# Kernel optimization log

Hardware: AMD Instinct MI355X
Metric: run time of the kernel (lower is better)

## Reference

```python
import jax, jax.numpy as jnp
import numpy as np

# Module constants derived from default grid_config
D = 59          # depth bins: (60-1)/1
C_OUT = 64
X, Y, Z = 128, 128, 7
STRIDE = 16
GRID_LB = np.array([-51.2, -51.2, -2.5], dtype=np.float32)
GRID_IV = np.array([0.8, 0.8, 1.0], dtype=np.float32)
D0, DSTEP = 1.0, 1.0

B, N, C_IN, H, W = 4, 6, 256, 16, 44


def _voxel_coords():
    xs, ys, zs = np.meshgrid(np.arange(X), np.arange(Y), np.arange(Z), indexing='ij')
    coords = np.stack([xs, ys, zs], axis=-1).reshape(-1, 3).astype(np.float32)
    coords = coords * GRID_IV + GRID_LB  # [V, 3] ego-frame voxel centers
    return coords


def _camera_rig(rng):
    """Realistic 6-camera rig: yawed cameras looking outward, z_cam = forward."""
    c2e = np.zeros((B, N, 4, 4), dtype=np.float32)
    K = np.zeros((B, N, 3, 3), dtype=np.float32)
    for b in range(B):
        for n in range(N):
            a = 2.0 * np.pi * n / N + 0.02 * rng.standard_normal()
            f = np.array([np.cos(a), np.sin(a), 0.0])           # camera forward (z_cam)
            x_cam = np.array([-np.sin(a), np.cos(a), 0.0])      # camera right
            y_cam = np.array([0.0, 0.0, -1.0])                   # camera down
            R = np.stack([x_cam, y_cam, f], axis=1)              # columns = cam axes in ego
            t = 1.0 * f + np.array([0.0, 0.0, 1.5])
            c2e[b, n, :3, :3] = R
            c2e[b, n, :3, 3] = t
            c2e[b, n, 3, 3] = 1.0
            fl = 400.0 + 5.0 * rng.standard_normal()
            K[b, n] = np.array([[fl, 0.0, 352.0], [0.0, fl, 128.0], [0.0, 0.0, 1.0]])
    return c2e, K


def setup_inputs() -> dict:
    key = jax.random.key(0)
    k1, k2, k3 = jax.random.split(key, 3)
    img_feats = jax.random.normal(k1, (B, N, C_IN, H, W), dtype=jnp.float32)
    c2e, K = _camera_rig(np.random.default_rng(0))
    # depth_net: 1x1 conv in_channels -> D + C_OUT
    w_depth = jax.random.normal(k2, (D + C_OUT, C_IN), dtype=jnp.float32) * (1.0 / np.sqrt(C_IN))
    b_depth = jax.random.normal(k3, (D + C_OUT,), dtype=jnp.float32) * 0.01
    return {
        'img_feats': img_feats,
        'cam2ego': jnp.asarray(c2e),
        'cam_intrinsics': jnp.asarray(K),
        'w_depth': w_depth,
        'b_depth': b_depth,
    }


def reference(img_feats, cam2ego, cam_intrinsics, w_depth, b_depth):
    Bc, Nc, C, Hc, Wc = img_feats.shape
    # 1x1 conv == per-pixel linear
    x = jnp.einsum('bnchw,oc->bnhwo', img_feats, w_depth) + b_depth  # [B,N,H,W,D+C_OUT]
    depth = jax.nn.softmax(x[..., :D], axis=-1)                      # [B,N,H,W,D]
    feat = x[..., D:]                                                # [B,N,H,W,C_OUT]

    vox = jnp.asarray(_voxel_coords())                               # [V,3]
    V = vox.shape[0]
    vox_h = jnp.concatenate([vox, jnp.ones((V, 1), vox.dtype)], axis=1)  # [V,4]

    e2c = jnp.linalg.inv(cam2ego)                                    # [B,N,4,4]
    cam = jnp.einsum('bnij,vj->bnvi', e2c, vox_h)[..., :3]           # [B,N,V,3]
    z = cam[..., 2]
    z_safe = jnp.maximum(z, 0.1)
    norm = cam[..., :2] / z_safe[..., None]
    homo = jnp.concatenate([norm, jnp.ones_like(z[..., None])], axis=-1)  # [B,N,V,3]
    img = jnp.einsum('bnij,bnvj->bnvi', cam_intrinsics, homo)[..., :2]
    fc = img / STRIDE                                                # feature-plane coords

    depth_bin = ((z - D0) / DSTEP).astype(jnp.int32)                 # trunc toward 0, matches .long()
    valid = (
        (fc[..., 0] >= 0) & (fc[..., 0] < Wc)
        & (fc[..., 1] >= 0) & (fc[..., 1] < Hc)
        & (z > 0.5)
        & (depth_bin >= 0) & (depth_bin < D)
    )

    u = jnp.clip(fc[..., 0].astype(jnp.int32), 0, Wc - 1)            # [B,N,V]
    v = jnp.clip(fc[..., 1].astype(jnp.int32), 0, Hc - 1)
    d = jnp.clip(depth_bin, 0, D - 1)
    hw = v * Wc + u

    feat_flat = feat.reshape(Bc, Nc, Hc * Wc, C_OUT)
    sampled_feat = jnp.take_along_axis(feat_flat, hw[..., None], axis=2)   # [B,N,V,C_OUT]
    depth_flat = depth.reshape(Bc, Nc, Hc * Wc * D)
    sampled_depth = jnp.take_along_axis(depth_flat, hw * D + d, axis=2)    # [B,N,V]

    wgt = sampled_depth * valid.astype(sampled_depth.dtype)
    # scatter_add at flat_idx == voxel index (identity) -> masked sum over cameras
    bev = jnp.einsum('bnv,bnvc->bvc', wgt, sampled_feat)             # [B,V,C_OUT]
    bev = bev.reshape(Bc, X, Y, Z, C_OUT).sum(axis=3)                # collapse Z
    bev = bev.transpose(0, 3, 2, 1)                                  # [B,C_OUT,Y,X]
    return bev, depth
```

## Files before the change

kernel.cpp:

```cpp
#include <hip/hip_runtime.h>
#include <math.h>

#define D_BINS 59
#define CO     64
#define CI     256
#define NB     4
#define NC     6
#define H_IMG  16
#define W_IMG  44
#define HW     704
#define NPIX   (NB*NC*HW)
#define XD     128
#define YD     128
#define ZD     7
#define NOUT   123
#define PXB    66

typedef float v2f __attribute__((ext_vector_type(2)));

__device__ void inv_rigid(const float* __restrict__ M, float* __restrict__ o) {
    double a = M[0], b = M[1], c = M[2], t0 = M[3];
    double d = M[4], e = M[5], f = M[6], t1 = M[7];
    double g = M[8], h = M[9], ii = M[10], t2 = M[11];
    double A00 = e*ii - f*h, A01 = c*h - b*ii, A02 = b*f - c*e;
    double A10 = f*g - d*ii, A11 = a*ii - c*g, A12 = c*d - a*f;
    double A20 = d*h - e*g,  A21 = b*g - a*h,  A22 = a*e - b*d;
    double det = a*A00 + b*A10 + c*A20;
    double inv = 1.0 / det;
    double r00 = A00*inv, r01 = A01*inv, r02 = A02*inv;
    double r10 = A10*inv, r11 = A11*inv, r12 = A12*inv;
    double r20 = A20*inv, r21 = A21*inv, r22 = A22*inv;
    o[0] = (float)r00; o[1] = (float)r01; o[2]  = (float)r02;
    o[3] = (float)(-(r00*t0 + r01*t1 + r02*t2));
    o[4] = (float)r10; o[5] = (float)r11; o[6]  = (float)r12;
    o[7] = (float)(-(r10*t0 + r11*t1 + r12*t2));
    o[8] = (float)r20; o[9] = (float)r21; o[10] = (float)r22;
    o[11] = (float)(-(r20*t0 + r21*t1 + r22*t2));
}

__global__ __launch_bounds__(256) void k_pre(
    const float* __restrict__ wd, const float* __restrict__ c2e,
    float* __restrict__ wt2, float* __restrict__ e2c) {
    const int o = blockIdx.x;
    const int k = threadIdx.x;
    float v = (o < NOUT) ? wd[(size_t)o * CI + k] : 0.f;
    wt2[(size_t)(k >> 1) * 256 + o * 2 + (k & 1)] = v;
    if (blockIdx.x == 0 && k < NB * NC)
        inv_rigid(c2e + k * 16, e2c + k * 12);
}

__global__ __launch_bounds__(640) void k_head(
    const float* __restrict__ img, const float* __restrict__ wt2,
    const float* __restrict__ bd, float* __restrict__ depth_out,
    float* __restrict__ feat_ws) {
    __shared__ float smem[PXB * 132 + PXB];
    float* S = smem + PXB * 132;

    const int tid = threadIdx.x;
    const int wv  = tid >> 6;
    const int ln  = tid & 63;
    const int p0  = blockIdx.x * PXB;
    const bool is_main = (wv < 8);
    const int o0  = __builtin_amdgcn_readfirstlane((is_main ? wv : 0) << 4);
    const int epx = 64 + (wv - 8);

    v2f acc[16];
#pragma unroll
    for (int j = 0; j < 16; ++j) acc[j] = (v2f)(0.f);
    v2f acc2a = (v2f)(0.f), acc2b = (v2f)(0.f);

    for (int kc = 0; kc < 4; ++kc) {
#pragma unroll
        for (int it = 0; it < 7; ++it) {
            int idx = tid + it * 640;
            if (idx < 64 * PXB) {
                int kl = idx / PXB, px = idx - kl * PXB;
                int p = p0 + px;
                int bn = p / HW, hw = p - bn * HW;
                smem[(kl >> 1) * 132 + px * 2 + (kl & 1)] =
                    img[((size_t)bn * CI + kc * 64 + kl) * HW + hw];
            }
        }
        __syncthreads();
        if (is_main) {
#pragma unroll 4
            for (int k2 = 0; k2 < 32; ++k2) {
                v2f a = *(const v2f*)(smem + k2 * 132 + ln * 2);
                const v2f* w =
                    (const v2f*)(wt2 + (size_t)(kc * 32 + k2) * 256) + o0;
#pragma unroll
                for (int j = 0; j < 16; ++j)
                    acc[j] = __builtin_elementwise_fma(a, w[j], acc[j]);
            }
        } else {
#pragma unroll 4
            for (int k2 = 0; k2 < 32; ++k2) {
                v2f a = *(const v2f*)(smem + k2 * 132 + epx * 2);
                const float* w = wt2 + (size_t)(kc * 32 + k2) * 256;
                v2f w0 = {w[ln * 2], w[ln * 2 + 1]};
                v2f w1 = {w[(ln + 64) * 2], w[(ln + 64) * 2 + 1]};
                acc2a = __builtin_elementwise_fma(a, w0, acc2a);
                acc2b = __builtin_elementwise_fma(a, w1, acc2b);
            }
        }
        __syncthreads();
    }

    float* X = smem;
    if (is_main) {
#pragma unroll
        for (int j = 0; j < 16; ++j) {
            int o = o0 + j;
            if (o < NOUT) {
                int col = (o < D_BINS) ? o : o + 5;
                X[ln * 132 + col] = (acc[j].x + acc[j].y) + bd[o];
            }
        }
    } else {
        int o = ln;
        X[epx * 132 + ((o < D_BINS) ? o : o + 5)] = (acc2a.x + acc2a.y) + bd[o];
        o = ln + 64;
        if (o < NOUT)
            X[epx * 132 + ((o < D_BINS) ? o : o + 5)] = (acc2b.x + acc2b.y) + bd[o];
    }
    __syncthreads();

#pragma unroll
    for (int it = 0; it < 2; ++it) {
        int g = tid + it * 640;
        if (g < PXB * 16) {
            int p = g >> 4, m = g & 15;
            float4 v = *(const float4*)(X + p * 132 + 64 + m * 4);
            *(float4*)(feat_ws + (size_t)(p0 + p) * CO + m * 4) = v;
        }
    }

    if (tid < PXB) {
        float* row = X + tid * 132;
        float m = row[0];
        for (int o = 1; o < D_BINS; ++o) m = fmaxf(m, row[o]);
        float s = 0.f;
        for (int o = 0; o < D_BINS; ++o) {
            float e = __expf(row[o] - m);
            row[o] = e;
            s += e;
        }
        S[tid] = 1.f / s;
    }
    __syncthreads();

    for (int g = tid; g < PXB * D_BINS; g += 640) {
        int p = g / D_BINS;
        int o = g - p * D_BINS;
        depth_out[(size_t)p0 * D_BINS + g] = X[p * 132 + o] * S[p];
    }
}

__global__ __launch_bounds__(256) void k_splat(
    const float* __restrict__ e2c, const float* __restrict__ Kmat,
    const float* __restrict__ depth_g, const float* __restrict__ feat_ws,
    float* __restrict__ bev) {
    __shared__ int   hw_s[ZD][64];
    __shared__ float wgt_s[ZD][64];

    const int tx = threadIdx.x;
    const int cq = threadIdx.y;
    const int x = blockIdx.x * 64 + tx;
    const int y = blockIdx.y;
    const int b = blockIdx.z;
    const float wx = (float)x * 0.8f + (-51.2f);
    const float wy = (float)y * 0.8f + (-51.2f);

    float acc[16];
#pragma unroll
    for (int m = 0; m < 16; ++m) acc[m] = 0.f;

    for (int n = 0; n < NC; ++n) {
        const int bn = b * NC + n;
        const float* E = e2c + bn * 12;
        const float* Km = Kmat + bn * 9;
        const float k00 = Km[0], k01 = Km[1], k02 = Km[2];
        const float k10 = Km[3], k11 = Km[4], k12 = Km[5];
        const float e02 = E[2], e12 = E[6], e22 = E[10];
        const float bx0 = E[0] * wx + E[1] * wy + E[3];
        const float bx1 = E[4] * wx + E[5] * wy + E[7];
        const float bx2 = E[8] * wx + E[9] * wy + E[11];

#pragma unroll
        for (int zz = 0; zz < 2; ++zz) {
            const int z = cq + zz * 4;
            if (z < ZD) {
                const float wz = -2.5f + (float)z;
                const float cx = bx0 + e02 * wz;
                const float cy = bx1 + e12 * wz;
                const float cz = bx2 + e22 * wz;
                const float zs = fmaxf(cz, 0.1f);
                const float rz = 1.0f / zs;
                const float xn = cx * rz;
                const float yn = cy * rz;
                const float fu = (k00 * xn + k01 * yn + k02) * 0.0625f;
                const float fv = (k10 * xn + k11 * yn + k12) * 0.0625f;
                const int bin = (int)(cz - 1.0f);
                const bool valid = (fu >= 0.f) & (fu < (float)W_IMG) &
                                   (fv >= 0.f) & (fv < (float)H_IMG) &
                                   (cz > 0.5f) & (bin >= 0) & (bin < D_BINS);
                int hw = -1;
                float wgt = 0.f;
                if (valid) {
                    int u = (int)fu;
                    int v = (int)fv;
                    hw = v * W_IMG + u;
                    wgt = depth_g[((size_t)bn * HW + hw) * D_BINS + bin];
                }
                hw_s[z][tx] = hw;
                wgt_s[z][tx] = wgt;
            }
        }
        __syncthreads();

#pragma unroll
        for (int z = 0; z < ZD; ++z) {
            const int hw = hw_s[z][tx];
            if (hw >= 0) {
                const float wgt = wgt_s[z][tx];
                const float4* fp =
                    (const float4*)(feat_ws + ((size_t)bn * HW + hw) * CO + cq * 16);
                float4 f0 = fp[0], f1 = fp[1], f2 = fp[2], f3 = fp[3];
                acc[0]  = fmaf(wgt, f0.x, acc[0]);
                acc[1]  = fmaf(wgt, f0.y, acc[1]);
                acc[2]  = fmaf(wgt, f0.z, acc[2]);
                acc[3]  = fmaf(wgt, f0.w, acc[3]);
                acc[4]  = fmaf(wgt, f1.x, acc[4]);
                acc[5]  = fmaf(wgt, f1.y, acc[5]);
                acc[6]  = fmaf(wgt, f1.z, acc[6]);
                acc[7]  = fmaf(wgt, f1.w, acc[7]);
                acc[8]  = fmaf(wgt, f2.x, acc[8]);
                acc[9]  = fmaf(wgt, f2.y, acc[9]);
                acc[10] = fmaf(wgt, f2.z, acc[10]);
                acc[11] = fmaf(wgt, f2.w, acc[11]);
                acc[12] = fmaf(wgt, f3.x, acc[12]);
                acc[13] = fmaf(wgt, f3.y, acc[13]);
                acc[14] = fmaf(wgt, f3.z, acc[14]);
                acc[15] = fmaf(wgt, f3.w, acc[15]);
            }
        }
        __syncthreads();
    }
    float* ob = bev + (((size_t)b * CO + cq * 16) * YD + y) * XD + x;
#pragma unroll
    for (int m = 0; m < 16; ++m) ob[(size_t)m * YD * XD] = acc[m];
}

extern "C" void kernel_launch(void* const* d_in, const int* in_sizes, int n_in,
                              void* d_out, int out_size, void* d_ws, size_t ws_size,
                              hipStream_t stream) {
    const float* img  = (const float*)d_in[0];
    const float* c2e  = (const float*)d_in[1];
    const float* Kmat = (const float*)d_in[2];
    const float* wd   = (const float*)d_in[3];
    const float* bd   = (const float*)d_in[4];
    float* bev = (float*)d_out;
    float* depth_out = bev + (size_t)NB * CO * YD * XD;
    float* feat_ws = (float*)d_ws;
    float* wt2 = feat_ws + (size_t)NPIX * CO;
    float* e2c = wt2 + 128 * 256;

    k_pre<<<128, 256, 0, stream>>>(wd, c2e, wt2, e2c);
    k_head<<<256, 640, 0, stream>>>(img, wt2, bd, depth_out, feat_ws);
    k_splat<<<dim3(2, YD, NB), dim3(64, 4, 1), 0, stream>>>(e2c, Kmat, depth_out,
                                                            feat_ws, bev);
}
```

Baseline: 124.0 us.

## Retile depth-head GEMM into 32-pixel blocks with split-K across waves

Rewrites the 1x1-conv head kernel to process 32 pixels per 256-thread block, loading all 256 input channels into shared memory at once. Each lane owns two output channels and sixteen pixels, and two wave pairs split the K dimension, reducing their partials through LDS. The grid grows from 256 to 528 blocks for better CU coverage, and the irregular 66-pixel tile with special-case extra waves is removed. In exchange there is more weight traffic per pixel from global memory and a larger shared-memory footprint.

```diff
diff --git a/kernel.cpp b/kernel.cpp
--- a/kernel.cpp
+++ b/kernel.cpp
@@ -14,7 +14,8 @@
 #define YD     128
 #define ZD     7
 #define NOUT   123
-#define PXB    66
+#define PXT    32
+#define XW     132
 
 typedef float v2f __attribute__((ext_vector_type(2)));
 
@@ -49,94 +50,83 @@
         inv_rigid(c2e + k * 16, e2c + k * 12);
 }
 
-__global__ __launch_bounds__(640) void k_head(
+__global__ __launch_bounds__(256) void k_head(
     const float* __restrict__ img, const float* __restrict__ wt2,
     const float* __restrict__ bd, float* __restrict__ depth_out,
     float* __restrict__ feat_ws) {
-    __shared__ float smem[PXB * 132 + PXB];
-    float* S = smem + PXB * 132;
+    __shared__ float A[128 * 64];
+    __shared__ float Xs[PXT * XW];
+    __shared__ float S[PXT];
 
     const int tid = threadIdx.x;
     const int wv  = tid >> 6;
     const int ln  = tid & 63;
-    const int p0  = blockIdx.x * PXB;
-    const bool is_main = (wv < 8);
-    const int o0  = __builtin_amdgcn_readfirstlane((is_main ? wv : 0) << 4);
-    const int epx = 64 + (wv - 8);
-
-    v2f acc[16];
-#pragma unroll
-    for (int j = 0; j < 16; ++j) acc[j] = (v2f)(0.f);
-    v2f acc2a = (v2f)(0.f), acc2b = (v2f)(0.f);
-
-    for (int kc = 0; kc < 4; ++kc) {
-#pragma unroll
-        for (int it = 0; it < 7; ++it) {
-            int idx = tid + it * 640;
-            if (idx < 64 * PXB) {
-                int kl = idx / PXB, px = idx - kl * PXB;
-                int p = p0 + px;
-                int bn = p / HW, hw = p - bn * HW;
-                smem[(kl >> 1) * 132 + px * 2 + (kl & 1)] =
-                    img[((size_t)bn * CI + kc * 64 + kl) * HW + hw];
-            }
-        }
-        __syncthreads();
-        if (is_main) {
-#pragma unroll 4
-            for (int k2 = 0; k2 < 32; ++k2) {
-                v2f a = *(const v2f*)(smem + k2 * 132 + ln * 2);
-                const v2f* w =
-                    (const v2f*)(wt2 + (size_t)(kc * 32 + k2) * 256) + o0;
-#pragma unroll
-                for (int j = 0; j < 16; ++j)
-                    acc[j] = __builtin_elementwise_fma(a, w[j], acc[j]);
-            }
-        } else {
-#pragma unroll 4
-            for (int k2 = 0; k2 < 32; ++k2) {
-                v2f a = *(const v2f*)(smem + k2 * 132 + epx * 2);
-                const float* w = wt2 + (size_t)(kc * 32 + k2) * 256;
-                v2f w0 = {w[ln * 2], w[ln * 2 + 1]};
-                v2f w1 = {w[(ln + 64) * 2], w[(ln + 64) * 2 + 1]};
-                acc2a = __builtin_elementwise_fma(a, w0, acc2a);
-                acc2b = __builtin_elementwise_fma(a, w1, acc2b);
-            }
-        }
-        __syncthreads();
-    }
-
-    float* X = smem;
-    if (is_main) {
-#pragma unroll
-        for (int j = 0; j < 16; ++j) {
-            int o = o0 + j;
-            if (o < NOUT) {
-                int col = (o < D_BINS) ? o : o + 5;
-                X[ln * 132 + col] = (acc[j].x + acc[j].y) + bd[o];
-            }
-        }
-    } else {
-        int o = ln;
-        X[epx * 132 + ((o < D_BINS) ? o : o + 5)] = (acc2a.x + acc2a.y) + bd[o];
-        o = ln + 64;
-        if (o < NOUT)
-            X[epx * 132 + ((o < D_BINS) ? o : o + 5)] = (acc2b.x + acc2b.y) + bd[o];
-    }
-    __syncthreads();
-
-#pragma unroll
-    for (int it = 0; it < 2; ++it) {
-        int g = tid + it * 640;
-        if (g < PXB * 16) {
-            int p = g >> 4, m = g & 15;
-            float4 v = *(const float4*)(X + p * 132 + 64 + m * 4);
-            *(float4*)(feat_ws + (size_t)(p0 + p) * CO + m * 4) = v;
-        }
-    }
-
-    if (tid < PXB) {
-        float* row = X + tid * 132;
+    const int p0  = blockIdx.x * PXT;
+    const int pw0 = (wv & 1) << 4;
+    const int kh  = wv >> 1;
+    const int kb  = __builtin_amdgcn_readfirstlane(kh << 6);
+
+    const int bn  = p0 / HW;
+    const int hw0 = p0 - bn * HW;
+    const float* gsrc = img + (size_t)bn * CI * HW + hw0;
+#pragma unroll 8
+    for (int it = 0; it < 32; ++it) {
+        int idx = tid + it * 256;
+        int ch = idx >> 5, px = idx & 31;
+        A[(ch >> 1) * 64 + px * 2 + (ch & 1)] = gsrc[ch * HW + px];
+    }
+    __syncthreads();
+
+    v2f accA[16], accB[16];
+#pragma unroll
+    for (int p = 0; p < 16; ++p) { accA[p] = (v2f)(0.f); accB[p] = (v2f)(0.f); }
+
+#pragma unroll 2
+    for (int k2i = 0; k2i < 64; ++k2i) {
+        const int k2 = kb + k2i;
+        float4 w4 = *(const float4*)(wt2 + (size_t)k2 * 256 + ln * 4);
+        v2f wA = {w4.x, w4.y};
+        v2f wB = {w4.z, w4.w};
+        const float* ar = A + k2 * 64 + pw0 * 2;
+#pragma unroll
+        for (int i = 0; i < 8; ++i) {
+            float4 aq = *(const float4*)(ar + i * 4);
+            v2f a0 = {aq.x, aq.y};
+            v2f a1 = {aq.z, aq.w};
+            accA[2*i]   = __builtin_elementwise_fma(a0, wA, accA[2*i]);
+            accB[2*i]   = __builtin_elementwise_fma(a0, wB, accB[2*i]);
+            accA[2*i+1] = __builtin_elementwise_fma(a1, wA, accA[2*i+1]);
+            accB[2*i+1] = __builtin_elementwise_fma(a1, wB, accB[2*i+1]);
+        }
+    }
+
+    if (kh == 0) {
+#pragma unroll
+        for (int p = 0; p < 16; ++p) {
+            v2f v = { accA[p].x + accA[p].y, accB[p].x + accB[p].y };
+            *(v2f*)(Xs + (pw0 + p) * XW + 2 * ln) = v;
+        }
+    }
+    __syncthreads();
+    if (kh == 1) {
+        float b0 = (2 * ln     < NOUT) ? bd[2 * ln]     : 0.f;
+        float b1 = (2 * ln + 1 < NOUT) ? bd[2 * ln + 1] : 0.f;
+#pragma unroll
+        for (int p = 0; p < 16; ++p) {
+            v2f s = *(const v2f*)(Xs + (pw0 + p) * XW + 2 * ln);
+            v2f v = { (s.x + (accA[p].x + accA[p].y)) + b0,
+                      (s.y + (accB[p].x + accB[p].y)) + b1 };
+            *(v2f*)(Xs + (pw0 + p) * XW + 2 * ln) = v;
+        }
+    }
+    __syncthreads();
+
+    for (int g = tid; g < PXT * CO; g += 256) {
+        int p = g >> 6, c = g & 63;
+        feat_ws[(size_t)(p0 + p) * CO + c] = Xs[p * XW + 59 + c];
+    }
+    if (tid < PXT) {
+        float* row = Xs + tid * XW;
         float m = row[0];
         for (int o = 1; o < D_BINS; ++o) m = fmaxf(m, row[o]);
         float s = 0.f;
@@ -148,11 +138,10 @@
         S[tid] = 1.f / s;
     }
     __syncthreads();
-
-    for (int g = tid; g < PXB * D_BINS; g += 640) {
+    for (int g = tid; g < PXT * D_BINS; g += 256) {
         int p = g / D_BINS;
         int o = g - p * D_BINS;
-        depth_out[(size_t)p0 * D_BINS + g] = X[p * 132 + o] * S[p];
+        depth_out[(size_t)p0 * D_BINS + g] = Xs[p * XW + o] * S[p];
     }
 }
 
@@ -266,7 +255,7 @@
     float* e2c = wt2 + 128 * 256;
 
     k_pre<<<128, 256, 0, stream>>>(wd, c2e, wt2, e2c);
-    k_head<<<256, 640, 0, stream>>>(img, wt2, bd, depth_out, feat_ws);
+    k_head<<<528, 256, 0, stream>>>(img, wt2, bd, depth_out, feat_ws);
     k_splat<<<dim3(2, YD, NB), dim3(64, 4, 1), 0, stream>>>(e2c, Kmat, depth_out,
                                                             feat_ws, bev);
 }
```

Measured after the change: 125.0 us. About the same (+0.8%).

## Compute depth-net head GEMM with split-bf16 MFMA instead of FP32 FMAs

Applied to the files above, without the earlier changes.

The 1x1 conv head now runs on bf16 MFMA instructions (16x16x32). Weights and image features are split into hi/lo bf16 pairs, and three MFMA products are summed to approximate FP32 accuracy. Image features are staged once into XOR-swizzled shared memory, replacing the four-chunk K loop, and the block shrinks to 512 threads. This removes the scalar FP32 FMA bottleneck, at the cost of a small precision loss from the bf16x3 emulation and a larger shared-memory footprint.

```diff
diff --git a/kernel.cpp b/kernel.cpp
--- a/kernel.cpp
+++ b/kernel.cpp
@@ -16,7 +16,17 @@
 #define NOUT   123
 #define PXB    66
 
-typedef float v2f __attribute__((ext_vector_type(2)));
+typedef float v2f  __attribute__((ext_vector_type(2)));
+typedef short short8 __attribute__((ext_vector_type(8)));
+typedef float f32x4  __attribute__((ext_vector_type(4)));
+
+__device__ inline unsigned short f2bf(float f) {
+    unsigned u = __float_as_uint(f);
+    return (unsigned short)((u + 0x7FFFu + ((u >> 16) & 1u)) >> 16);
+}
+__device__ inline float bf2f(unsigned short h) {
+    return __uint_as_float((unsigned)h << 16);
+}
 
 __device__ void inv_rigid(const float* __restrict__ M, float* __restrict__ o) {
     double a = M[0], b = M[1], c = M[2], t0 = M[3];
@@ -40,99 +50,99 @@
 
 __global__ __launch_bounds__(256) void k_pre(
     const float* __restrict__ wd, const float* __restrict__ c2e,
-    float* __restrict__ wt2, float* __restrict__ e2c) {
+    unsigned short* __restrict__ whi, unsigned short* __restrict__ wlo,
+    float* __restrict__ e2c) {
     const int o = blockIdx.x;
     const int k = threadIdx.x;
-    float v = (o < NOUT) ? wd[(size_t)o * CI + k] : 0.f;
-    wt2[(size_t)(k >> 1) * 256 + o * 2 + (k & 1)] = v;
+    float f = (o < NOUT) ? wd[(size_t)o * CI + k] : 0.f;
+    unsigned short hi = f2bf(f);
+    whi[o * 256 + k] = hi;
+    wlo[o * 256 + k] = f2bf(f - bf2f(hi));
     if (blockIdx.x == 0 && k < NB * NC)
         inv_rigid(c2e + k * 16, e2c + k * 12);
 }
 
-__global__ __launch_bounds__(640) void k_head(
-    const float* __restrict__ img, const float* __restrict__ wt2,
-    const float* __restrict__ bd, float* __restrict__ depth_out,
-    float* __restrict__ feat_ws) {
-    __shared__ float smem[PXB * 132 + PXB];
-    float* S = smem + PXB * 132;
+__global__ __launch_bounds__(512) void k_head(
+    const float* __restrict__ img, const unsigned short* __restrict__ whi_g,
+    const unsigned short* __restrict__ wlo_g, const float* __restrict__ bd,
+    float* __restrict__ depth_out, float* __restrict__ feat_ws) {
+    __shared__ __align__(16) unsigned short Bbuf[2 * PXB * 256];
+    __shared__ float S[PXB];
+    unsigned short* BH = Bbuf;
+    unsigned short* BL = Bbuf + PXB * 256;
 
     const int tid = threadIdx.x;
     const int wv  = tid >> 6;
     const int ln  = tid & 63;
+    const int lm  = ln & 15;
+    const int lg  = ln >> 4;
     const int p0  = blockIdx.x * PXB;
-    const bool is_main = (wv < 8);
-    const int o0  = __builtin_amdgcn_readfirstlane((is_main ? wv : 0) << 4);
-    const int epx = 64 + (wv - 8);
-
-    v2f acc[16];
-#pragma unroll
-    for (int j = 0; j < 16; ++j) acc[j] = (v2f)(0.f);
-    v2f acc2a = (v2f)(0.f), acc2b = (v2f)(0.f);
-
-    for (int kc = 0; kc < 4; ++kc) {
-#pragma unroll
-        for (int it = 0; it < 7; ++it) {
-            int idx = tid + it * 640;
-            if (idx < 64 * PXB) {
-                int kl = idx / PXB, px = idx - kl * PXB;
-                int p = p0 + px;
-                int bn = p / HW, hw = p - bn * HW;
-                smem[(kl >> 1) * 132 + px * 2 + (kl & 1)] =
-                    img[((size_t)bn * CI + kc * 64 + kl) * HW + hw];
+
+    for (int it = 0; it < 33; ++it) {
+        int idx = tid + it * 512;
+        int c = idx / PXB, px = idx - c * PXB;
+        int p = p0 + px;
+        int bn = p / HW, hw = p - bn * HW;
+        float f = img[((size_t)bn * CI + c) * HW + hw];
+        unsigned short hi = f2bf(f);
+        unsigned short lo = f2bf(f - bf2f(hi));
+        int si = (px * 256 + c) ^ ((px & 7) << 3);
+        BH[si] = hi;
+        BL[si] = lo;
+    }
+    __syncthreads();
+
+    f32x4 acc[5];
+#pragma unroll
+    for (int t = 0; t < 5; ++t) acc[t] = (f32x4)(0.f);
+
+    int pxs[5];
+#pragma unroll
+    for (int t = 0; t < 4; ++t) pxs[t] = t * 16 + lm;
+    pxs[4] = (lm < 2) ? (64 + lm) : 65;
+
+    const unsigned short* wh = whi_g + (size_t)(wv * 16 + lm) * 256;
+    const unsigned short* wl = wlo_g + (size_t)(wv * 16 + lm) * 256;
+
+#pragma unroll
+    for (int s = 0; s < 8; ++s) {
+        const int kk = s * 32 + lg * 8;
+        short8 a_hi = *(const short8*)(wh + kk);
+        short8 a_lo = *(const short8*)(wl + kk);
+#pragma unroll
+        for (int t = 0; t < 5; ++t) {
+            int si = (pxs[t] * 256 + kk) ^ ((pxs[t] & 7) << 3);
+            short8 b_hi = *(const short8*)(BH + si);
+            short8 b_lo = *(const short8*)(BL + si);
+            acc[t] = __builtin_amdgcn_mfma_f32_16x16x32_bf16(a_hi, b_hi, acc[t], 0, 0, 0);
+            acc[t] = __builtin_amdgcn_mfma_f32_16x16x32_bf16(a_hi, b_lo, acc[t], 0, 0, 0);
+            acc[t] = __builtin_amdgcn_mfma_f32_16x16x32_bf16(a_lo, b_hi, acc[t], 0, 0, 0);
+        }
+    }
+    __syncthreads();
+
+    float* X = (float*)Bbuf;
+    const int ob = wv * 16 + lg * 4;
+#pragma unroll
+    for (int t = 0; t < 5; ++t) {
+        int px = t * 16 + lm;
+        if (px < PXB) {
+#pragma unroll
+            for (int r = 0; r < 4; ++r) {
+                int o = ob + r;
+                if (o < NOUT) {
+                    int col = (o < D_BINS) ? o : o + 5;
+                    X[px * 132 + col] = acc[t][r] + bd[o];
+                }
             }
         }
-        __syncthreads();
-        if (is_main) {
-#pragma unroll 4
-            for (int k2 = 0; k2 < 32; ++k2) {
-                v2f a = *(const v2f*)(smem + k2 * 132 + ln * 2);
-                const v2f* w =
-                    (const v2f*)(wt2 + (size_t)(kc * 32 + k2) * 256) + o0;
-#pragma unroll
-                for (int j = 0; j < 16; ++j)
-                    acc[j] = __builtin_elementwise_fma(a, w[j], acc[j]);
-            }
-        } else {
-#pragma unroll 4
-            for (int k2 = 0; k2 < 32; ++k2) {
-                v2f a = *(const v2f*)(smem + k2 * 132 + epx * 2);
-                const float* w = wt2 + (size_t)(kc * 32 + k2) * 256;
-                v2f w0 = {w[ln * 2], w[ln * 2 + 1]};
-                v2f w1 = {w[(ln + 64) * 2], w[(ln + 64) * 2 + 1]};
-                acc2a = __builtin_elementwise_fma(a, w0, acc2a);
-                acc2b = __builtin_elementwise_fma(a, w1, acc2b);
-            }
-        }
-        __syncthreads();
-    }
-
-    float* X = smem;
-    if (is_main) {
-#pragma unroll
-        for (int j = 0; j < 16; ++j) {
-            int o = o0 + j;
-            if (o < NOUT) {
-                int col = (o < D_BINS) ? o : o + 5;
-                X[ln * 132 + col] = (acc[j].x + acc[j].y) + bd[o];
-            }
-        }
-    } else {
-        int o = ln;
-        X[epx * 132 + ((o < D_BINS) ? o : o + 5)] = (acc2a.x + acc2a.y) + bd[o];
-        o = ln + 64;
-        if (o < NOUT)
-            X[epx * 132 + ((o < D_BINS) ? o : o + 5)] = (acc2b.x + acc2b.y) + bd[o];
-    }
-    __syncthreads();
-
-#pragma unroll
-    for (int it = 0; it < 2; ++it) {
-        int g = tid + it * 640;
-        if (g < PXB * 16) {
-            int p = g >> 4, m = g & 15;
-            float4 v = *(const float4*)(X + p * 132 + 64 + m * 4);
-            *(float4*)(feat_ws + (size_t)(p0 + p) * CO + m * 4) = v;
-        }
+    }
+    __syncthreads();
+
+    for (int g = tid; g < PXB * 16; g += 512) {
+        int p = g >> 4, m = g & 15;
+        float4 v = *(const float4*)(X + p * 132 + 64 + m * 4);
+        *(float4*)(feat_ws + (size_t)(p0 + p) * CO + m * 4) = v;
     }
 
     if (tid < PXB) {
@@ -149,7 +159,7 @@
     }
     __syncthreads();
 
-    for (int g = tid; g < PXB * D_BINS; g += 640) {
+    for (int g = tid; g < PXB * D_BINS; g += 512) {
         int p = g / D_BINS;
         int o = g - p * D_BINS;
         depth_out[(size_t)p0 * D_BINS + g] = X[p * 132 + o] * S[p];
@@ -262,11 +272,12 @@
     float* bev = (float*)d_out;
     float* depth_out = bev + (size_t)NB * CO * YD * XD;
     float* feat_ws = (float*)d_ws;
-    float* wt2 = feat_ws + (size_t)NPIX * CO;
-    float* e2c = wt2 + 128 * 256;
-
-    k_pre<<<128, 256, 0, stream>>>(wd, c2e, wt2, e2c);
-    k_head<<<256, 640, 0, stream>>>(img, wt2, bd, depth_out, feat_ws);
+    unsigned short* whi = (unsigned short*)(feat_ws + (size_t)NPIX * CO);
+    unsigned short* wlo = whi + 128 * 256;
+    float* e2c = (float*)(wlo + 128 * 256);
+
+    k_pre<<<128, 256, 0, stream>>>(wd, c2e, whi, wlo, e2c);
+    k_head<<<256, 512, 0, stream>>>(img, whi, wlo, bd, depth_out, feat_ws);
     k_splat<<<dim3(2, YD, NB), dim3(64, 4, 1), 0, stream>>>(e2c, Kmat, depth_out,
                                                             feat_ws, bev);
 }
```

Result: faster. 120.9 us (-2.5%).
